# Kernel optimization log

Hardware: AMD Instinct MI355X
Metric: run time of the kernel (lower is better)

## Reference

```python
import jax, jax.numpy as jnp
import numpy as np

IN_DIMS = 4
DEPTH = 4
C = IN_DIMS + 1                     # channels after time augmentation
SIG = sum(C ** k for k in range(1, DEPTH + 1))  # 780
N, T = 64, 1024


def setup_inputs() -> dict:
    key = jax.random.key(0)
    k1, k2, k3, k4, k5 = jax.random.split(key, 5)
    batch = jax.random.normal(k1, (N, T, IN_DIMS), dtype=jnp.float32)
    s_c = 1.0 / np.sqrt(C)
    conv_w = jax.random.normal(k2, (C, C), dtype=jnp.float32) * s_c
    conv_b = jax.random.normal(k3, (C,), dtype=jnp.float32) * s_c
    s_l = 1.0 / np.sqrt(SIG)
    lin_w = jax.random.normal(k4, (SIG, SIG), dtype=jnp.float32) * s_l
    lin_b = jax.random.normal(k5, (SIG,), dtype=jnp.float32) * s_l
    return {"batch": batch, "conv_w": conv_w, "conv_b": conv_b,
            "lin_w": lin_w, "lin_b": lin_b}


def _stream_signature(path):
    """Streamed path signature with zero basepoint.

    path: (n, t, C). Returns (n, t, SIG) where entry t is the signature of
    the piecewise-linear path (0, path[0], ..., path[t]) truncated at DEPTH,
    levels flattened in lexicographic (row-major) order like signatory.
    """
    n = path.shape[0]
    # increments; basepoint=True means first increment is path[:,0] - 0
    dx = jnp.concatenate([path[:, :1, :], path[:, 1:, :] - path[:, :-1, :]], axis=1)
    init = tuple(jnp.zeros((n, C ** k), path.dtype) for k in range(1, DEPTH + 1))

    def step(levels, d):
        # exp(d) in the truncated tensor algebra: e_k = d^{(x)k} / k!
        e = [d]
        for k in range(2, DEPTH + 1):
            e.append((jnp.einsum('na,nb->nab', e[-1], d) / k).reshape(n, -1))
        # Chen: new_k = e_k + S_k + sum_{i=1}^{k-1} S_i (x) e_{k-i}
        new = []
        for k in range(1, DEPTH + 1):
            acc = levels[k - 1] + e[k - 1]
            for i in range(1, k):
                acc = acc + jnp.einsum('na,nb->nab', levels[i - 1], e[k - i - 1]).reshape(n, -1)
            new.append(acc)
        new = tuple(new)
        return new, jnp.concatenate(new, axis=-1)

    _, ys = jax.lax.scan(step, init, jnp.swapaxes(dx, 0, 1))  # ys: (t, n, SIG)
    return jnp.swapaxes(ys, 0, 1)


def reference(batch, conv_w, conv_b, lin_w, lin_b):
    n, t, _ = batch.shape
    # time augmentation: append channel arange(1,T+1)/T
    time = (jnp.arange(1, t + 1, dtype=batch.dtype) / t)[None, :, None]
    a = jnp.concatenate([batch, jnp.broadcast_to(time, (n, t, 1))], axis=-1)  # (n,t,C)
    # kernel-size-1 conv1d == pointwise linear over channels
    b = a @ conv_w.T + conv_b                                                  # (n,t,C)
    c = _stream_signature(b)                                                   # (n,t,SIG)
    # zero out the first stream entry (torch.concat of zeros with c[:,1:,:])
    c = jnp.concatenate([jnp.zeros((n, 1, SIG), c.dtype), c[:, 1:, :]], axis=1)
    return jnp.tanh(c @ lin_w.T + lin_b)
```

## Files before the change

### kernel.cpp

```cpp
#include <hip/hip_runtime.h>
#include <math.h>

#define N_B 64
#define T_LEN 1024
#define IN_D 4
#define CH 5
#define SIG 780
#define KP 800
#define NPAD 896
#define SEG_LEN 16
#define N_SEG 64
#define SC_L1 1.0f
#define SC_L2 0.25f
#define SC_L3 0.0625f
#define SC_L4 0.015625f

typedef _Float16 f16x8 __attribute__((ext_vector_type(8)));
typedef float f32x4 __attribute__((ext_vector_type(4)));

typedef __attribute__((address_space(1))) const void* as1cp;
typedef __attribute__((address_space(3))) void* as3p;

__device__ __forceinline__ float fast_tanh(float x) {
  float ax = fabsf(x);
  float e = __expf(-2.0f * ax);
  float r = (1.0f - e) * __builtin_amdgcn_rcpf(1.0f + e);
  return copysignf(r, x);
}

__device__ __forceinline__ float sel5(float d0, float d1, float d2, float d3,
                                      float d4, int i) {
  float r = d0;
  r = (i == 1) ? d1 : r;
  r = (i == 2) ? d2 : r;
  r = (i == 3) ? d3 : r;
  r = (i == 4) ? d4 : r;
  return r;
}


__global__ __launch_bounds__(64) void seg_wave(
    const float* __restrict__ batch,
    const float* __restrict__ conv_w,
    const float* __restrict__ conv_b,
    float* __restrict__ P) {
  int s = blockIdx.x;
  int n = blockIdx.y;
  int lane = threadIdx.x;

  __shared__ float S123[160];
  __shared__ float bc[85];
  __shared__ float dsh[SEG_LEN][CH];

  for (int i = lane; i < 160; i += 64) S123[i] = 0.0f;
#pragma unroll
  for (int p = 0; p < 2; ++p) {
    int e = lane + p * 64;
    if (e < (SEG_LEN + 1) * CH) {
      int r = s * SEG_LEN - 1 + e / CH, ch = e % CH;
      float v = 0.0f;
      if (r >= 0) {
        const float* a = batch + ((size_t)n * T_LEN + r) * IN_D;
        const float* w = conv_w + ch * CH;
        v = conv_b[ch];
        v = fmaf(a[0], w[0], v);
        v = fmaf(a[1], w[1], v);
        v = fmaf(a[2], w[2], v);
        v = fmaf(a[3], w[3], v);
        v = fmaf((float)(r + 1) * (1.0f / T_LEN), w[4], v);
      }
      bc[e] = v;
    }
  }
  __syncthreads();
#pragma unroll
  for (int p = 0; p < 2; ++p) {
    int e = lane + p * 64;
    if (e < SEG_LEN * CH) dsh[e / CH][e % CH] = bc[e + CH] - bc[e];
  }
  __syncthreads();

  const int xb = lane * 10;
  const int a_lo = xb / 125, a_hi = (xb + 9) / 125;
  const int s2_lo = xb / 25, s2_hi = (xb + 9) / 25;
  const int s3_lo = 2 * lane, s3_hi = 2 * lane + 1;
  const int b_lo = s2_lo % 5, b_hi = s2_hi % 5;
  const int c_lo = s3_lo % 5, c_hi = s3_hi % 5;
  const int q_a = a_lo * 125 + 125 - xb;
  const int q_b = s2_lo * 25 + 25 - xb;
  const int y0 = lane, y1 = lane + 64;
  const bool hy0 = (y0 < 125), hy1 = (y1 < 125);
  const int y0a = y0 / 25, y0s = y0 / 5, y0b = y0s % 5, y0c = y0 % 5;
  const int y1a = y1 / 25, y1s = y1 / 5, y1b = y1s % 5, y1c = y1 % 5;
  const bool hz = (lane < 25);
  const int za = lane / 5, zb = lane % 5;
  const bool h1 = (lane < 5);

  float S4r[10];
#pragma unroll
  for (int q = 0; q < 10; ++q) S4r[q] = 0.0f;

  for (int j = 0; j < SEG_LEN; ++j) {
    float dr0 = dsh[j][0], dr1 = dsh[j][1], dr2 = dsh[j][2], dr3 = dsh[j][3],
          dr4 = dsh[j][4];
    float drA[5] = {dr0, dr1, dr2, dr3, dr4};
    float da_l = sel5(dr0, dr1, dr2, dr3, dr4, a_lo);
    float da_h = sel5(dr0, dr1, dr2, dr3, dr4, a_hi);
    float db_l = sel5(dr0, dr1, dr2, dr3, dr4, b_lo);
    float db_h = sel5(dr0, dr1, dr2, dr3, dr4, b_hi);
    float dc_l = sel5(dr0, dr1, dr2, dr3, dr4, c_lo);
    float dc_h = sel5(dr0, dr1, dr2, dr3, dr4, c_hi);
    float s1_l = S123[a_lo], s1_h = S123[a_hi];
    float s2v_l = S123[5 + s2_lo], s2v_h = S123[5 + s2_hi];
    float s3v_l = S123[30 + s3_lo], s3v_h = S123[30 + s3_hi];

#pragma unroll
    for (int q = 0; q < 10; ++q) {
      bool ua = (q >= q_a), ub = (q >= q_b);
      float s1 = ua ? s1_h : s1_l, da = ua ? da_h : da_l;
      float s2v = ub ? s2v_h : s2v_l, db = ub ? db_h : db_l;
      float s3v = (q < 5) ? s3v_l : s3v_h;
      float dc = (q < 5) ? dc_l : dc_h;
      float dd = drA[q % 5];
      float tH = fmaf(0.25f, da, s1);
      tH = fmaf((1.0f / 3.0f) * db, tH, s2v);
      tH = fmaf(0.5f * dc, tH, s3v);
      S4r[q] = fmaf(dd, tH, S4r[q]);
    }

    float n3_0 = 0.f, n3_1 = 0.f, n2 = 0.f, n1 = 0.f;
    if (hy0) {
      float tH = fmaf((1.0f / 3.0f), drA[0] * 0.f + dsh[j][y0a], S123[y0a]);
      tH = fmaf(0.5f * dsh[j][y0b], tH, S123[5 + y0s]);
      n3_0 = fmaf(dsh[j][y0c], tH, S123[30 + y0]);
    }
    if (hy1) {
      float tH = fmaf((1.0f / 3.0f), dsh[j][y1a], S123[y1a]);
      tH = fmaf(0.5f * dsh[j][y1b], tH, S123[5 + y1s]);
      n3_1 = fmaf(dsh[j][y1c], tH, S123[30 + y1]);
    }
    if (hz) {
      float tH = fmaf(0.5f, dsh[j][za], S123[za]);
      n2 = fmaf(dsh[j][zb], tH, S123[5 + lane]);
    }
    if (h1) n1 = S123[lane] + dsh[j][lane];
    __syncthreads();
    if (hy0) S123[30 + y0] = n3_0;
    if (hy1) S123[30 + y1] = n3_1;
    if (hz) S123[5 + lane] = n2;
    if (h1) S123[lane] = n1;
    __syncthreads();
  }

  float* Pr = P + ((size_t)n * N_SEG + s) * SIG;
  for (int i = lane; i < 155; i += 64) Pr[i] = S123[i];
#pragma unroll
  for (int q = 0; q < 10; ++q) {
    int x = xb + q;
    if (x < 625) Pr[155 + x] = S4r[q];
  }
}

__global__ __launch_bounds__(640) void prefix_kernel(float* __restrict__ P) {
  int n = blockIdx.x;
  int tid = threadIdx.x;
  __shared__ float A[SIG];
  __shared__ float Bs[SIG];

  float* Pn = P + (size_t)n * N_SEG * SIG;
  for (int i = tid; i < SIG; i += 640) A[i] = Pn[i];
  int i0 = tid, i1 = tid + 640;
  float r0 = 0.f, r1 = 0.f;
  if (i0 < SIG) r0 = Pn[SIG + i0];
  if (i1 < SIG) r1 = Pn[SIG + i1];

  const int e4 = tid;
  const int q4a = e4 / 125, r125 = e4 % 125, r25 = e4 % 25, r5 = e4 % 5;
  const int e4d5 = e4 / 5, e4d25 = e4 / 25;
  const int e3 = tid;
  const int e3a = e3 / 25, e3r25 = e3 % 25, e3r5 = e3 % 5, e3d5 = e3 / 5;
  const int e2 = tid - 125;
  const int e1 = tid - 150;

  for (int s = 1; s < N_SEG; ++s) {
    if (i0 < SIG) Bs[i0] = r0;
    if (i1 < SIG) Bs[i1] = r1;
    __syncthreads();
    if (s + 1 < N_SEG) {
      const float* Pnx = Pn + (size_t)(s + 1) * SIG;
      if (i0 < SIG) r0 = Pnx[i0];
      if (i1 < SIG) r1 = Pnx[i1];
    }
    float v4 = 0.f, v3 = 0.f, v2 = 0.f, v1 = 0.f;
    if (tid < 625) {
      v4 = A[155 + e4] + Bs[155 + e4];
      v4 = fmaf(A[30 + e4d5], Bs[r5], v4);
      v4 = fmaf(A[5 + e4d25], Bs[5 + r25], v4);
      v4 = fmaf(A[q4a], Bs[30 + r125], v4);
    }
    if (tid < 125) {
      v3 = A[30 + e3] + Bs[30 + e3];
      v3 = fmaf(A[5 + e3d5], Bs[e3r5], v3);
      v3 = fmaf(A[e3a], Bs[5 + e3r25], v3);
    } else if (tid < 150) {
      v2 = A[5 + e2] + Bs[5 + e2];
      v2 = fmaf(A[e2 / 5], Bs[e2 % 5], v2);
    } else if (tid < 155) {
      v1 = A[e1] + Bs[e1];
    }
    __syncthreads();
    float* Po = Pn + (size_t)s * SIG;
    if (tid < 625) { A[155 + e4] = v4; Po[155 + e4] = v4; }
    if (tid < 125) { A[30 + e3] = v3; Po[30 + e3] = v3; }
    else if (tid < 150) { A[5 + e2] = v2; Po[5 + e2] = v2; }
    else if (tid < 155) { A[e1] = v1; Po[e1] = v1; }
  }
}

__global__ __launch_bounds__(64) void emit_wave(
    const float* __restrict__ batch,
    const float* __restrict__ conv_w,
    const float* __restrict__ conv_b,
    const float* __restrict__ P,
    _Float16* __restrict__ c1,
    _Float16* __restrict__ c2) {
  int s = blockIdx.x;
  int n = blockIdx.y;
  int lane = threadIdx.x;

  __shared__ float S123[160];
  __shared__ float bc[85];
  __shared__ float dsh[SEG_LEN][CH];
  __shared__ __align__(16) _Float16 row1[KP];
  __shared__ __align__(16) _Float16 row2[KP];

  const int xb = lane * 10;
  float S4r[10];
  if (s == 0) {
    for (int i = lane; i < 160; i += 64) S123[i] = 0.0f;
#pragma unroll
    for (int q = 0; q < 10; ++q) S4r[q] = 0.0f;
  } else {
    const float* Pr = P + ((size_t)n * N_SEG + (s - 1)) * SIG;
    for (int i = lane; i < 155; i += 64) S123[i] = Pr[i];
    if (lane < 5) S123[155 + lane] = 0.0f;
#pragma unroll
    for (int q = 0; q < 10; ++q) {
      int x = xb + q;
      S4r[q] = (x < 625) ? Pr[155 + x] : 0.0f;
    }
  }
#pragma unroll
  for (int p = 0; p < 2; ++p) {
    int e = lane + p * 64;
    if (e < (SEG_LEN + 1) * CH) {
      int r = s * SEG_LEN - 1 + e / CH, ch = e % CH;
      float v = 0.0f;
      if (r >= 0) {
        const float* a = batch + ((size_t)n * T_LEN + r) * IN_D;
        const float* w = conv_w + ch * CH;
        v = conv_b[ch];
        v = fmaf(a[0], w[0], v);
        v = fmaf(a[1], w[1], v);
        v = fmaf(a[2], w[2], v);
        v = fmaf(a[3], w[3], v);
        v = fmaf((float)(r + 1) * (1.0f / T_LEN), w[4], v);
      }
      bc[e] = v;
    }
  }
  if (lane < KP - SIG) {
    row1[SIG + lane] = (_Float16)0.0f;
    row2[SIG + lane] = (_Float16)0.0f;
  }
  __syncthreads();
#pragma unroll
  for (int p = 0; p < 2; ++p) {
    int e = lane + p * 64;
    if (e < SEG_LEN * CH) dsh[e / CH][e % CH] = bc[e + CH] - bc[e];
  }
  __syncthreads();

  const int a_lo = xb / 125, a_hi = (xb + 9) / 125;
  const int s2_lo = xb / 25, s2_hi = (xb + 9) / 25;
  const int s3_lo = 2 * lane, s3_hi = 2 * lane + 1;
  const int b_lo = s2_lo % 5, b_hi = s2_hi % 5;
  const int c_lo = s3_lo % 5, c_hi = s3_hi % 5;
  const int q_a = a_lo * 125 + 125 - xb;
  const int q_b = s2_lo * 25 + 25 - xb;
  const int y0 = lane, y1 = lane + 64;
  const bool hy0 = (y0 < 125), hy1 = (y1 < 125);
  const int y0a = y0 / 25, y0s = y0 / 5, y0b = y0s % 5, y0c = y0 % 5;
  const int y1a = y1 / 25, y1s = y1 / 5, y1b = y1s % 5, y1c = y1 % 5;
  const bool hz = (lane < 25);
  const int za = lane / 5, zb = lane % 5;
  const bool h1 = (lane < 5);

  for (int j = 0; j < SEG_LEN; ++j) {
    int t = s * SEG_LEN + j;
    float zf = (t == 0) ? 0.0f : 1.0f;
    float dr0 = dsh[j][0], dr1 = dsh[j][1], dr2 = dsh[j][2], dr3 = dsh[j][3],
          dr4 = dsh[j][4];
    float drA[5] = {dr0, dr1, dr2, dr3, dr4};
    float da_l = sel5(dr0, dr1, dr2, dr3, dr4, a_lo);
    float da_h = sel5(dr0, dr1, dr2, dr3, dr4, a_hi);
    float db_l = sel5(dr0, dr1, dr2, dr3, dr4, b_lo);
    float db_h = sel5(dr0, dr1, dr2, dr3, dr4, b_hi);
    float dc_l = sel5(dr0, dr1, dr2, dr3, dr4, c_lo);
    float dc_h = sel5(dr0, dr1, dr2, dr3, dr4, c_hi);
    float s1_l = S123[a_lo], s1_h = S123[a_hi];
    float s2v_l = S123[5 + s2_lo], s2v_h = S123[5 + s2_hi];
    float s3v_l = S123[30 + s3_lo], s3v_h = S123[30 + s3_hi];

#pragma unroll
    for (int q = 0; q < 10; ++q) {
      bool ua = (q >= q_a), ub = (q >= q_b);
      float s1 = ua ? s1_h : s1_l, da = ua ? da_h : da_l;
      float s2v = ub ? s2v_h : s2v_l, db = ub ? db_h : db_l;
      float s3v = (q < 5) ? s3v_l : s3v_h;
      float dc = (q < 5) ? dc_l : dc_h;
      float dd = drA[q % 5];
      float tH = fmaf(0.25f, da, s1);
      tH = fmaf((1.0f / 3.0f) * db, tH, s2v);
      tH = fmaf(0.5f * dc, tH, s3v);
      S4r[q] = fmaf(dd, tH, S4r[q]);
    }

    float n3_0 = 0.f, n3_1 = 0.f, n2 = 0.f, n1 = 0.f;
    if (hy0) {
      float tH = fmaf((1.0f / 3.0f), dsh[j][y0a], S123[y0a]);
      tH = fmaf(0.5f * dsh[j][y0b], tH, S123[5 + y0s]);
      n3_0 = fmaf(dsh[j][y0c], tH, S123[30 + y0]);
    }
    if (hy1) {
      float tH = fmaf((1.0f / 3.0f), dsh[j][y1a], S123[y1a]);
      tH = fmaf(0.5f * dsh[j][y1b], tH, S123[5 + y1s]);
      n3_1 = fmaf(dsh[j][y1c], tH, S123[30 + y1]);
    }
    if (hz) {
      float tH = fmaf(0.5f, dsh[j][za], S123[za]);
      n2 = fmaf(dsh[j][zb], tH, S123[5 + lane]);
    }
    if (h1) n1 = S123[lane] + dsh[j][lane];
    __syncthreads();

    if (hy0) S123[30 + y0] = n3_0;
    if (hy1) S123[30 + y1] = n3_1;
    if (hz) S123[5 + lane] = n2;
    if (h1) S123[lane] = n1;
#pragma unroll
    for (int q = 0; q < 10; ++q) {
      int x = xb + q;
      if (x < 625) {
        float v = S4r[q] * (SC_L4 * zf);
        _Float16 h = (_Float16)v;
        row1[155 + x] = h;
        row2[155 + x] = (_Float16)(v - (float)h);
      }
    }
    if (hy0) {
      float v = n3_0 * (SC_L3 * zf);
      _Float16 h = (_Float16)v;
      row1[30 + y0] = h; row2[30 + y0] = (_Float16)(v - (float)h);
    }
    if (hy1) {
      float v = n3_1 * (SC_L3 * zf);
      _Float16 h = (_Float16)v;
      row1[30 + y1] = h; row2[30 + y1] = (_Float16)(v - (float)h);
    }
    if (hz) {
      float v = n2 * (SC_L2 * zf);
      _Float16 h = (_Float16)v;
      row1[5 + lane] = h; row2[5 + lane] = (_Float16)(v - (float)h);
    }
    if (h1) {
      float v = n1 * (SC_L1 * zf);
      _Float16 h = (_Float16)v;
      row1[lane] = h; row2[lane] = (_Float16)(v - (float)h);
    }
    __syncthreads();

    size_t base = ((size_t)n * T_LEN + t) * KP;
    *(float4*)(c1 + base + lane * 8) = *(const float4*)&row1[lane * 8];
    *(float4*)(c2 + base + lane * 8) = *(const float4*)&row2[lane * 8];
    if (lane < 36) {
      *(float4*)(c1 + base + (64 + lane) * 8) = *(const float4*)&row1[(64 + lane) * 8];
      *(float4*)(c2 + base + (64 + lane) * 8) = *(const float4*)&row2[(64 + lane) * 8];
    }
  }
}

__global__ __launch_bounds__(256) void wconv_kernel(
    const float* __restrict__ W,
    _Float16* __restrict__ w1,
    _Float16* __restrict__ w2) {
  int idx = blockIdx.x * blockDim.x + threadIdx.x;
  if (idx >= NPAD * KP) return;
  int nn = idx / KP, k = idx % KP;
  float v = 0.0f;
  if (nn < SIG && k < SIG) {
    float sc = (k < 5) ? 1.0f : (k < 30) ? 4.0f : (k < 155) ? 16.0f : 64.0f;
    v = W[(size_t)nn * SIG + k] * sc;
  }
  _Float16 h = (_Float16)v;
  w1[idx] = h;
  w2[idx] = (_Float16)(v - (float)h);
}

__global__ __launch_bounds__(256) void gemm_mfma(
    const _Float16* __restrict__ A1p, const _Float16* __restrict__ A2p,
    const _Float16* __restrict__ B1p, const _Float16* __restrict__ B2p,
    const float* __restrict__ bias, float* __restrict__ out) {
  __shared__ _Float16 Al[2][2][128 * 32];
  __shared__ _Float16 Bl[2][2][128 * 32];

  int tid = threadIdx.x;
  int lane = tid & 63, wid = tid >> 6;
  int wm = wid >> 1, wn = wid & 1;
  int m0 = blockIdx.x * 128;

  int sr = lane >> 2, scn = lane & 3;
  int swst = (sr ^ (sr >> 2)) & 3;
  int qg = scn ^ swst;
  int fr = lane & 15, fq = lane >> 4;
  int swf = (fr ^ (fr >> 2)) & 3;
  int fchunk = fq ^ swf;

  auto stage = [&](int n0, int kb, int buf) {
    int k0 = kb * 32;
#pragma unroll
    for (int i = 0; i < 2; ++i) {
      int rloc = wid * 16 + i * 64 + sr;
      size_t gA = (size_t)(m0 + rloc) * KP + k0 + qg * 8;
      size_t gB = (size_t)(n0 + rloc) * KP + k0 + qg * 8;
      int lb = (wid * 16 + i * 64) * 32;
      __builtin_amdgcn_global_load_lds((as1cp)(A1p + gA), (as3p)(&Al[buf][0][lb]), 16, 0, 0);
      __builtin_amdgcn_global_load_lds((as1cp)(A2p + gA), (as3p)(&Al[buf][1][lb]), 16, 0, 0);
      __builtin_amdgcn_global_load_lds((as1cp)(B1p + gB), (as3p)(&Bl[buf][0][lb]), 16, 0, 0);
      __builtin_amdgcn_global_load_lds((as1cp)(B2p + gB), (as3p)(&Bl[buf][1][lb]), 16, 0, 0);
    }
  };

  for (int nt = 0; nt < 7; ++nt) {
    int n0 = nt * 128;

    f32x4 acc[4][4];
#pragma unroll
    for (int i = 0; i < 4; ++i)
#pragma unroll
      for (int j = 0; j < 4; ++j) acc[i][j] = (f32x4){0.f, 0.f, 0.f, 0.f};

    stage(n0, 0, 0);
    for (int kb = 0; kb < 25; ++kb) {
      int cur = kb & 1;
      __syncthreads();
      f16x8 a1[4], a2[4], b1[4], b2[4];
#pragma unroll
      for (int tm = 0; tm < 4; ++tm) {
        int off = (wm * 64 + tm * 16 + fr) * 32 + fchunk * 8;
        a1[tm] = *(const f16x8*)&Al[cur][0][off];
        a2[tm] = *(const f16x8*)&Al[cur][1][off];
      }
#pragma unroll
      for (int tn = 0; tn < 4; ++tn) {
        int off = (wn * 64 + tn * 16 + fr) * 32 + fchunk * 8;
        b1[tn] = *(const f16x8*)&Bl[cur][0][off];
        b2[tn] = *(const f16x8*)&Bl[cur][1][off];
      }
      if (kb < 24) stage(n0, kb + 1, cur ^ 1);
#pragma unroll
      for (int tm = 0; tm < 4; ++tm)
#pragma unroll
        for (int tn = 0; tn < 4; ++tn) {
          acc[tm][tn] = __builtin_amdgcn_mfma_f32_16x16x32_f16(a1[tm], b1[tn], acc[tm][tn], 0, 0, 0);
          acc[tm][tn] = __builtin_amdgcn_mfma_f32_16x16x32_f16(a1[tm], b2[tn], acc[tm][tn], 0, 0, 0);
          acc[tm][tn] = __builtin_amdgcn_mfma_f32_16x16x32_f16(a2[tm], b1[tn], acc[tm][tn], 0, 0, 0);
        }
    }
    __syncthreads();

    float* ep = (float*)((wid < 2) ? (void*)&Al[0][0][0] : (void*)&Bl[0][0][0]);
    ep += (wid & 1) * 4096;

    float bv[4];
#pragma unroll
    for (int tn = 0; tn < 4; ++tn) {
      int nn = n0 + wn * 64 + tn * 16 + fr;
      bv[tn] = (nn < SIG) ? bias[nn] : 0.0f;
    }
#pragma unroll
    for (int h = 0; h < 2; ++h) {
#pragma unroll
      for (int tm2 = 0; tm2 < 2; ++tm2) {
        int tm = h * 2 + tm2;
#pragma unroll
        for (int tn = 0; tn < 4; ++tn) {
#pragma unroll
          for (int r = 0; r < 4; ++r) {
            int lr = tm2 * 16 + fq * 4 + r;
            int lc = tn * 16 + fr;
            ep[lr * 66 + lc] = fast_tanh(acc[tm][tn][r] + bv[tn]);
          }
        }
      }
#pragma unroll
      for (int p = 0; p < 2; ++p) {
        int lr = lane & 31;
        int ck = (lane >> 5) * 2 + p;
        int gm = m0 + wm * 64 + h * 32 + lr;
        int gc0 = n0 + wn * 64 + ck * 16;
#pragma unroll
        for (int q = 0; q < 4; ++q) {
          int col = gc0 + q * 4;
          if (col + 3 < SIG) {
            *(float4*)(out + (size_t)gm * SIG + col) =
                *(const float4*)&ep[lr * 66 + ck * 16 + q * 4];
          } else if (col < SIG) {
#pragma unroll
            for (int e = 0; e < 4; ++e) {
              int c2 = col + e;
              if (c2 < SIG) out[(size_t)gm * SIG + c2] = ep[lr * 66 + ck * 16 + q * 4 + e];
            }
          }
        }
      }
    }
    __syncthreads();
  }
}

__global__ __launch_bounds__(256) void conv_kernel(
    const float* __restrict__ batch,
    const float* __restrict__ conv_w,
    const float* __restrict__ conv_b,
    float* __restrict__ b_out) {
  int idx = blockIdx.x * blockDim.x + threadIdx.x;
  if (idx >= N_B * T_LEN) return;
  int t = idx & (T_LEN - 1);
  const float* a = batch + (size_t)idx * IN_D;
  float a0 = a[0], a1 = a[1], a2 = a[2], a3 = a[3];
  float tm = (float)(t + 1) / (float)T_LEN;
  float* o = b_out + (size_t)idx * CH;
#pragma unroll
  for (int j = 0; j < CH; ++j) {
    const float* w = conv_w + j * CH;
    float r = conv_b[j];
    r = fmaf(tm, w[4], r);
    r = fmaf(a3, w[3], r);
    r = fmaf(a2, w[2], r);
    r = fmaf(a1, w[1], r);
    r = fmaf(a0, w[0], r);
    o[j] = r;
  }
}

__global__ __launch_bounds__(320) void sig_kernel_fb(
    const float* __restrict__ b_in, float* __restrict__ c_out) {
  int n = blockIdx.x;
  int tid = threadIdx.x;
  __shared__ float S[SIG];
  __shared__ float bc[64 * CH];
  __shared__ float dsh[CH];
  __shared__ float pb[CH];
  for (int i = tid; i < SIG; i += 320) S[i] = 0.0f;
  if (tid < CH) pb[tid] = 0.0f;
  const float* bn = b_in + (size_t)n * T_LEN * CH;
  float* cn = c_out + (size_t)n * T_LEN * SIG;
  const int x0 = tid, x1 = tid + 320;
  const bool has1 = (tid < 305);
  const int a0i = x0 / 125, b0i = (x0 / 25) % 5, c0i = (x0 / 5) % 5, d0i = x0 % 5;
  const int a1i = x1 / 125, b1i = (x1 / 25) % 5, c1i = (x1 / 5) % 5, d1i = x1 % 5;
  const int s2_0 = x0 / 25, s3_0 = x0 / 5, s2_1 = x1 / 25, s3_1 = x1 / 5;
  const bool hasL3 = (tid < 125);
  const int ya = tid / 25, yb = (tid / 5) % 5, yc = tid % 5;
  const bool hasL2 = (tid < 25);
  const int za = tid / 5, zb = tid % 5;
  const bool hasL1 = (tid < CH);
  for (int t = 0; t < T_LEN; ++t) {
    if ((t & 63) == 0) {
      __syncthreads();
      bc[tid] = bn[t * CH + tid];
      __syncthreads();
    }
    if (tid < CH) {
      float cur = bc[(t & 63) * CH + tid];
      dsh[tid] = cur - pb[tid];
      pb[tid] = cur;
    }
    __syncthreads();
    float n4_0, n4_1 = 0.0f, n3 = 0.0f, n2 = 0.0f, n1 = 0.0f;
    {
      float tH = fmaf(0.25f, dsh[a0i], S[a0i]);
      tH = fmaf((1.0f / 3.0f) * dsh[b0i], tH, S[5 + s2_0]);
      tH = fmaf(0.5f * dsh[c0i], tH, S[30 + s3_0]);
      n4_0 = fmaf(dsh[d0i], tH, S[155 + x0]);
    }
    if (has1) {
      float tH = fmaf(0.25f, dsh[a1i], S[a1i]);
      tH = fmaf((1.0f / 3.0f) * dsh[b1i], tH, S[5 + s2_1]);
      tH = fmaf(0.5f * dsh[c1i], tH, S[30 + s3_1]);
      n4_1 = fmaf(dsh[d1i], tH, S[155 + x1]);
    }
    if (hasL3) {
      float tH = fmaf((1.0f / 3.0f), dsh[ya], S[ya]);
      tH = fmaf(0.5f * dsh[yb], tH, S[5 + ya * 5 + yb]);
      n3 = fmaf(dsh[yc], tH, S[30 + tid]);
    }
    if (hasL2) {
      float tH = fmaf(0.5f, dsh[za], S[za]);
      n2 = fmaf(dsh[zb], tH, S[5 + tid]);
    }
    if (hasL1) n1 = S[tid] + dsh[tid];
    __syncthreads();
    S[155 + x0] = n4_0;
    if (has1) S[155 + x1] = n4_1;
    if (hasL3) S[30 + tid] = n3;
    if (hasL2) S[5 + tid] = n2;
    if (hasL1) S[tid] = n1;
    float* crow = cn + (size_t)t * SIG;
    float z = (t == 0) ? 0.0f : 1.0f;
    crow[155 + x0] = n4_0 * z;
    if (has1) crow[155 + x1] = n4_1 * z;
    if (hasL3) crow[30 + tid] = n3 * z;
    if (hasL2) crow[5 + tid] = n2 * z;
    if (hasL1) crow[tid] = n1 * z;
    __syncthreads();
  }
}

#define BM 256
#define BN 64
#define BK 16
__global__ __launch_bounds__(256) void gemm_tanh_fb(
    const float* __restrict__ Cmat, const float* __restrict__ W,
    const float* __restrict__ bias, float* __restrict__ out) {
  __shared__ float As[BK][BM + 4];
  __shared__ float Ws[BK][BN + 4];
  int tid = threadIdx.x;
  int tx = tid & 7, ty = tid >> 3;
  int m0 = blockIdx.x * BM, n0 = blockIdx.y * BN;
  float acc[8][8];
#pragma unroll
  for (int i = 0; i < 8; ++i)
#pragma unroll
    for (int j = 0; j < 8; ++j) acc[i][j] = 0.0f;
  for (int kb = 0; kb < SIG; kb += BK) {
    __syncthreads();
#pragma unroll
    for (int p = 0; p < 4; ++p) {
      int id = tid + p * 256;
      int row = id >> 2, kg = (id & 3) * 4, gk = kb + kg;
      float4 v = make_float4(0.f, 0.f, 0.f, 0.f);
      if (gk < SIG) v = *(const float4*)(Cmat + (size_t)(m0 + row) * SIG + gk);
      As[kg + 0][row] = v.x; As[kg + 1][row] = v.y;
      As[kg + 2][row] = v.z; As[kg + 3][row] = v.w;
    }
    {
      int row = tid >> 2, kg = (tid & 3) * 4, gk = kb + kg, wr = n0 + row;
      float4 v = make_float4(0.f, 0.f, 0.f, 0.f);
      if (gk < SIG && wr < SIG) v = *(const float4*)(W + (size_t)wr * SIG + gk);
      Ws[kg + 0][row] = v.x; Ws[kg + 1][row] = v.y;
      Ws[kg + 2][row] = v.z; Ws[kg + 3][row] = v.w;
    }
    __syncthreads();
#pragma unroll
    for (int k = 0; k < BK; ++k) {
      float af[8], wf[8];
      *(float4*)&af[0] = *(const float4*)&As[k][ty * 8];
      *(float4*)&af[4] = *(const float4*)&As[k][ty * 8 + 4];
      *(float4*)&wf[0] = *(const float4*)&Ws[k][tx * 8];
      *(float4*)&wf[4] = *(const float4*)&Ws[k][tx * 8 + 4];
#pragma unroll
      for (int i = 0; i < 8; ++i)
#pragma unroll
        for (int j = 0; j < 8; ++j) acc[i][j] = fmaf(af[i], wf[j], acc[i][j]);
    }
  }
#pragma unroll
  for (int i = 0; i < 8; ++i) {
    int m = m0 + ty * 8 + i;
    float* orow = out + (size_t)m * SIG;
#pragma unroll
    for (int jj = 0; jj < 8; jj += 4) {
      int col = n0 + tx * 8 + jj;
      if (col < SIG) {
        float4 r;
        r.x = tanhf(acc[i][jj + 0] + bias[col + 0]);
        r.y = tanhf(acc[i][jj + 1] + bias[col + 1]);
        r.z = tanhf(acc[i][jj + 2] + bias[col + 2]);
        r.w = tanhf(acc[i][jj + 3] + bias[col + 3]);
        *(float4*)(orow + col) = r;
      }
    }
  }
}

extern "C" void kernel_launch(void* const* d_in, const int* in_sizes, int n_in,
                              void* d_out, int out_size, void* d_ws, size_t ws_size,
                              hipStream_t stream) {
  const float* batch = (const float*)d_in[0];
  const float* conv_w = (const float*)d_in[1];
  const float* conv_b = (const float*)d_in[2];
  const float* lin_w = (const float*)d_in[3];
  const float* lin_b = (const float*)d_in[4];
  float* out = (float*)d_out;

  const size_t plane_elems = (size_t)N_B * T_LEN * KP;
  const size_t wplane_elems = (size_t)NPAD * KP;
  const size_t P_elems = (size_t)N_B * N_SEG * SIG;
  const size_t bp_elems = (size_t)N_B * T_LEN * CH;
  const size_t need_big = 2 * plane_elems * sizeof(_Float16) +
                          2 * wplane_elems * sizeof(_Float16) +
                          P_elems * sizeof(float);

  if (ws_size >= need_big) {
    _Float16* c1 = (_Float16*)d_ws;
    _Float16* c2 = c1 + plane_elems;
    _Float16* w1 = c2 + plane_elems;
    _Float16* w2 = w1 + wplane_elems;
    float* P = (float*)(w2 + wplane_elems);

    wconv_kernel<<<dim3((NPAD * KP + 255) / 256), dim3(256), 0, stream>>>(
        lin_w, w1, w2);
    seg_wave<<<dim3(N_SEG, N_B), dim3(64), 0, stream>>>(batch, conv_w, conv_b, P);
    prefix_kernel<<<dim3(N_B), dim3(640), 0, stream>>>(P);
    emit_wave<<<dim3(N_SEG, N_B), dim3(64), 0, stream>>>(
        batch, conv_w, conv_b, P, c1, c2);
    gemm_mfma<<<dim3(512), dim3(256), 0, stream>>>(c1, c2, w1, w2, lin_b, out);
  } else {
    float* b_path = (float*)d_ws;
    float* c_sig = (float*)d_ws + bp_elems;
    conv_kernel<<<dim3((N_B * T_LEN + 255) / 256), dim3(256), 0, stream>>>(
        batch, conv_w, conv_b, b_path);
    sig_kernel_fb<<<dim3(N_B), dim3(320), 0, stream>>>(b_path, c_sig);
    gemm_tanh_fb<<<dim3((N_B * T_LEN) / BM, (SIG + BN - 1) / BN), dim3(256), 0, stream>>>(
        c_sig, lin_w, lin_b, out);
  }
}
```

Before: 733.1 us.

## Pre-swizzle GEMM operands into MFMA fragment order and load directly to registers

emit_wave now buffers 16 timestep rows in LDS and writes the A operands (hi/lo f16 splits) in a blocked, MFMA-fragment-ordered layout. The weight conversion kernel writes B in the same order. The GEMM becomes gemm_direct: 3584 blocks, each computing one 128x128 output tile, loading fragments straight from global into registers with a software double buffer instead of staging through LDS with barriers. It also uses launch_bounds(256,2) and remaps blocks for locality. This removes LDS staging and syncs in the GEMM, but depends on global/L2 latency being hidden by the register double buffer, and raises emit_wave's LDS use.

```diff
diff --git a/kernel.cpp b/kernel.cpp
--- a/kernel.cpp
+++ b/kernel.cpp
@@ -10,6 +10,7 @@
 #define NPAD 896
 #define SEG_LEN 16
 #define N_SEG 64
+#define GBLK 51200
 #define SC_L1 1.0f
 #define SC_L2 0.25f
 #define SC_L3 0.0625f
@@ -17,9 +18,6 @@
 
 typedef _Float16 f16x8 __attribute__((ext_vector_type(8)));
 typedef float f32x4 __attribute__((ext_vector_type(4)));
-
-typedef __attribute__((address_space(1))) const void* as1cp;
-typedef __attribute__((address_space(3))) void* as3p;
 
 __device__ __forceinline__ float fast_tanh(float x) {
   float ax = fabsf(x);
@@ -37,7 +35,6 @@
   r = (i == 4) ? d4 : r;
   return r;
 }
-
 
 __global__ __launch_bounds__(64) void seg_wave(
     const float* __restrict__ batch,
@@ -130,7 +127,7 @@
 
     float n3_0 = 0.f, n3_1 = 0.f, n2 = 0.f, n1 = 0.f;
     if (hy0) {
-      float tH = fmaf((1.0f / 3.0f), drA[0] * 0.f + dsh[j][y0a], S123[y0a]);
+      float tH = fmaf((1.0f / 3.0f), dsh[j][y0a], S123[y0a]);
       tH = fmaf(0.5f * dsh[j][y0b], tH, S123[5 + y0s]);
       n3_0 = fmaf(dsh[j][y0c], tH, S123[30 + y0]);
     }
@@ -231,8 +228,7 @@
   __shared__ float S123[160];
   __shared__ float bc[85];
   __shared__ float dsh[SEG_LEN][CH];
-  __shared__ __align__(16) _Float16 row1[KP];
-  __shared__ __align__(16) _Float16 row2[KP];
+  __shared__ __align__(16) _Float16 rowbuf[2][16][808];
 
   const int xb = lane * 10;
   float S4r[10];
@@ -269,9 +265,9 @@
       bc[e] = v;
     }
   }
-  if (lane < KP - SIG) {
-    row1[SIG + lane] = (_Float16)0.0f;
-    row2[SIG + lane] = (_Float16)0.0f;
+  for (int i = lane; i < 2 * 16 * 20; i += 64) {
+    int p = i / 320, rr = (i / 20) % 16, cc = i % 20;
+    rowbuf[p][rr][780 + cc] = (_Float16)0.0f;
   }
   __syncthreads();
 #pragma unroll
@@ -348,184 +344,197 @@
     if (hy1) S123[30 + y1] = n3_1;
     if (hz) S123[5 + lane] = n2;
     if (h1) S123[lane] = n1;
+    _Float16* r1 = &rowbuf[0][j][0];
+    _Float16* r2 = &rowbuf[1][j][0];
 #pragma unroll
     for (int q = 0; q < 10; ++q) {
       int x = xb + q;
       if (x < 625) {
         float v = S4r[q] * (SC_L4 * zf);
         _Float16 h = (_Float16)v;
-        row1[155 + x] = h;
-        row2[155 + x] = (_Float16)(v - (float)h);
+        r1[155 + x] = h;
+        r2[155 + x] = (_Float16)(v - (float)h);
       }
     }
     if (hy0) {
       float v = n3_0 * (SC_L3 * zf);
       _Float16 h = (_Float16)v;
-      row1[30 + y0] = h; row2[30 + y0] = (_Float16)(v - (float)h);
+      r1[30 + y0] = h; r2[30 + y0] = (_Float16)(v - (float)h);
     }
     if (hy1) {
       float v = n3_1 * (SC_L3 * zf);
       _Float16 h = (_Float16)v;
-      row1[30 + y1] = h; row2[30 + y1] = (_Float16)(v - (float)h);
+      r1[30 + y1] = h; r2[30 + y1] = (_Float16)(v - (float)h);
     }
     if (hz) {
       float v = n2 * (SC_L2 * zf);
       _Float16 h = (_Float16)v;
-      row1[5 + lane] = h; row2[5 + lane] = (_Float16)(v - (float)h);
+      r1[5 + lane] = h; r2[5 + lane] = (_Float16)(v - (float)h);
     }
     if (h1) {
       float v = n1 * (SC_L1 * zf);
       _Float16 h = (_Float16)v;
-      row1[lane] = h; row2[lane] = (_Float16)(v - (float)h);
-    }
-    __syncthreads();
-
-    size_t base = ((size_t)n * T_LEN + t) * KP;
-    *(float4*)(c1 + base + lane * 8) = *(const float4*)&row1[lane * 8];
-    *(float4*)(c2 + base + lane * 8) = *(const float4*)&row2[lane * 8];
-    if (lane < 36) {
-      *(float4*)(c1 + base + (64 + lane) * 8) = *(const float4*)&row1[(64 + lane) * 8];
-      *(float4*)(c2 + base + (64 + lane) * 8) = *(const float4*)&row2[(64 + lane) * 8];
-    }
-  }
-}
-
-__global__ __launch_bounds__(256) void wconv_kernel(
+      r1[lane] = h; r2[lane] = (_Float16)(v - (float)h);
+    }
+    __syncthreads();
+  }
+
+  {
+    int g = n * 16 + (s >> 2);
+    int tm_r = s & 3;
+    int frl = lane & 15, fql = lane >> 4;
+    _Float16* d1 = c1 + (size_t)g * GBLK + tm_r * 512 + lane * 8;
+    _Float16* d2 = c2 + (size_t)g * GBLK + tm_r * 512 + lane * 8;
+#pragma unroll
+    for (int kb = 0; kb < 25; ++kb) {
+      *(f16x8*)(d1 + kb * 2048) = *(const f16x8*)&rowbuf[0][frl][kb * 32 + fql * 8];
+      *(f16x8*)(d2 + kb * 2048) = *(const f16x8*)&rowbuf[1][frl][kb * 32 + fql * 8];
+    }
+  }
+}
+
+__global__ __launch_bounds__(256) void wswz_kernel(
     const float* __restrict__ W,
     _Float16* __restrict__ w1,
     _Float16* __restrict__ w2) {
   int idx = blockIdx.x * blockDim.x + threadIdx.x;
-  if (idx >= NPAD * KP) return;
-  int nn = idx / KP, k = idx % KP;
+  if (idx >= 14 * GBLK) return;
+  int gn = idx / GBLK;
+  int r1 = idx % GBLK;
+  int kb = r1 / 2048;
+  int r2 = r1 % 2048;
+  int tn = r2 / 512;
+  int r3 = r2 % 512;
+  int fq = r3 / 128;
+  int fr = (r3 >> 3) & 15;
+  int jv = r3 & 7;
+  int nrow = gn * 64 + tn * 16 + fr;
+  int k = kb * 32 + fq * 8 + jv;
   float v = 0.0f;
-  if (nn < SIG && k < SIG) {
+  if (nrow < SIG && k < SIG) {
     float sc = (k < 5) ? 1.0f : (k < 30) ? 4.0f : (k < 155) ? 16.0f : 64.0f;
-    v = W[(size_t)nn * SIG + k] * sc;
+    v = W[(size_t)nrow * SIG + k] * sc;
   }
   _Float16 h = (_Float16)v;
   w1[idx] = h;
   w2[idx] = (_Float16)(v - (float)h);
 }
 
-__global__ __launch_bounds__(256) void gemm_mfma(
+__global__ __launch_bounds__(256, 2) void gemm_direct(
     const _Float16* __restrict__ A1p, const _Float16* __restrict__ A2p,
     const _Float16* __restrict__ B1p, const _Float16* __restrict__ B2p,
     const float* __restrict__ bias, float* __restrict__ out) {
-  __shared__ _Float16 Al[2][2][128 * 32];
-  __shared__ _Float16 Bl[2][2][128 * 32];
+  __shared__ float eplds[4][2112];
 
   int tid = threadIdx.x;
   int lane = tid & 63, wid = tid >> 6;
   int wm = wid >> 1, wn = wid & 1;
-  int m0 = blockIdx.x * 128;
-
-  int sr = lane >> 2, scn = lane & 3;
-  int swst = (sr ^ (sr >> 2)) & 3;
-  int qg = scn ^ swst;
+  int b = blockIdx.x;
+  int x = b & 7, jj = b >> 3;
+  int mstrip = x * 64 + jj / 7;
+  int nt = jj % 7;
+
+  int g = mstrip * 2 + wm;
+  int gn = nt * 2 + wn;
+
+  const _Float16* aB1 = A1p + (size_t)g * GBLK + lane * 8;
+  const _Float16* aB2 = A2p + (size_t)g * GBLK + lane * 8;
+  const _Float16* bB1 = B1p + (size_t)gn * GBLK + lane * 8;
+  const _Float16* bB2 = B2p + (size_t)gn * GBLK + lane * 8;
+
+  f32x4 acc[4][4];
+#pragma unroll
+  for (int i = 0; i < 4; ++i)
+#pragma unroll
+    for (int j = 0; j < 4; ++j) acc[i][j] = (f32x4){0.f, 0.f, 0.f, 0.f};
+
+  f16x8 aE1[4], aE2[4], bE1[4], bE2[4];
+  f16x8 aO1[4], aO2[4], bO1[4], bO2[4];
+
+  auto loadf = [&](int kb, f16x8* A1f, f16x8* A2f, f16x8* B1f, f16x8* B2f) {
+    int o = kb * 2048;
+#pragma unroll
+    for (int tt = 0; tt < 4; ++tt) {
+      A1f[tt] = *(const f16x8*)(aB1 + o + tt * 512);
+      A2f[tt] = *(const f16x8*)(aB2 + o + tt * 512);
+      B1f[tt] = *(const f16x8*)(bB1 + o + tt * 512);
+      B2f[tt] = *(const f16x8*)(bB2 + o + tt * 512);
+    }
+  };
+  auto domfma = [&](f16x8* A1f, f16x8* A2f, f16x8* B1f, f16x8* B2f) {
+#pragma unroll
+    for (int tm = 0; tm < 4; ++tm)
+#pragma unroll
+      for (int tn = 0; tn < 4; ++tn)
+        acc[tm][tn] = __builtin_amdgcn_mfma_f32_16x16x32_f16(A1f[tm], B1f[tn], acc[tm][tn], 0, 0, 0);
+#pragma unroll
+    for (int tm = 0; tm < 4; ++tm)
+#pragma unroll
+      for (int tn = 0; tn < 4; ++tn)
+        acc[tm][tn] = __builtin_amdgcn_mfma_f32_16x16x32_f16(A1f[tm], B2f[tn], acc[tm][tn], 0, 0, 0);
+#pragma unroll
+    for (int tm = 0; tm < 4; ++tm)
+#pragma unroll
+      for (int tn = 0; tn < 4; ++tn)
+        acc[tm][tn] = __builtin_amdgcn_mfma_f32_16x16x32_f16(A2f[tm], B1f[tn], acc[tm][tn], 0, 0, 0);
+  };
+
+  loadf(0, aE1, aE2, bE1, bE2);
+#pragma unroll 1
+  for (int i = 0; i < 12; ++i) {
+    loadf(2 * i + 1, aO1, aO2, bO1, bO2);
+    domfma(aE1, aE2, bE1, bE2);
+    loadf(2 * i + 2, aE1, aE2, bE1, bE2);
+    domfma(aO1, aO2, bO1, bO2);
+  }
+  domfma(aE1, aE2, bE1, bE2);
+
+  int m0 = mstrip * 128, n0 = nt * 128;
   int fr = lane & 15, fq = lane >> 4;
-  int swf = (fr ^ (fr >> 2)) & 3;
-  int fchunk = fq ^ swf;
-
-  auto stage = [&](int n0, int kb, int buf) {
-    int k0 = kb * 32;
-#pragma unroll
-    for (int i = 0; i < 2; ++i) {
-      int rloc = wid * 16 + i * 64 + sr;
-      size_t gA = (size_t)(m0 + rloc) * KP + k0 + qg * 8;
-      size_t gB = (size_t)(n0 + rloc) * KP + k0 + qg * 8;
-      int lb = (wid * 16 + i * 64) * 32;
-      __builtin_amdgcn_global_load_lds((as1cp)(A1p + gA), (as3p)(&Al[buf][0][lb]), 16, 0, 0);
-      __builtin_amdgcn_global_load_lds((as1cp)(A2p + gA), (as3p)(&Al[buf][1][lb]), 16, 0, 0);
-      __builtin_amdgcn_global_load_lds((as1cp)(B1p + gB), (as3p)(&Bl[buf][0][lb]), 16, 0, 0);
-      __builtin_amdgcn_global_load_lds((as1cp)(B2p + gB), (as3p)(&Bl[buf][1][lb]), 16, 0, 0);
-    }
-  };
-
-  for (int nt = 0; nt < 7; ++nt) {
-    int n0 = nt * 128;
-
-    f32x4 acc[4][4];
-#pragma unroll
-    for (int i = 0; i < 4; ++i)
-#pragma unroll
-      for (int j = 0; j < 4; ++j) acc[i][j] = (f32x4){0.f, 0.f, 0.f, 0.f};
-
-    stage(n0, 0, 0);
-    for (int kb = 0; kb < 25; ++kb) {
-      int cur = kb & 1;
-      __syncthreads();
-      f16x8 a1[4], a2[4], b1[4], b2[4];
-#pragma unroll
-      for (int tm = 0; tm < 4; ++tm) {
-        int off = (wm * 64 + tm * 16 + fr) * 32 + fchunk * 8;
-        a1[tm] = *(const f16x8*)&Al[cur][0][off];
-        a2[tm] = *(const f16x8*)&Al[cur][1][off];
+  float* ep = eplds[wid];
+
+  float bv[4];
+#pragma unroll
+  for (int tn = 0; tn < 4; ++tn) {
+    int nn = n0 + wn * 64 + tn * 16 + fr;
+    bv[tn] = (nn < SIG) ? bias[nn] : 0.0f;
+  }
+#pragma unroll
+  for (int h = 0; h < 2; ++h) {
+#pragma unroll
+    for (int tm2 = 0; tm2 < 2; ++tm2) {
+      int tm = h * 2 + tm2;
+#pragma unroll
+      for (int tn = 0; tn < 4; ++tn) {
+#pragma unroll
+        for (int r = 0; r < 4; ++r) {
+          int lr = tm2 * 16 + fq * 4 + r;
+          int lc = tn * 16 + fr;
+          ep[lr * 66 + lc] = fast_tanh(acc[tm][tn][r] + bv[tn]);
+        }
       }
-#pragma unroll
-      for (int tn = 0; tn < 4; ++tn) {
-        int off = (wn * 64 + tn * 16 + fr) * 32 + fchunk * 8;
-        b1[tn] = *(const f16x8*)&Bl[cur][0][off];
-        b2[tn] = *(const f16x8*)&Bl[cur][1][off];
-      }
-      if (kb < 24) stage(n0, kb + 1, cur ^ 1);
-#pragma unroll
-      for (int tm = 0; tm < 4; ++tm)
-#pragma unroll
-        for (int tn = 0; tn < 4; ++tn) {
-          acc[tm][tn] = __builtin_amdgcn_mfma_f32_16x16x32_f16(a1[tm], b1[tn], acc[tm][tn], 0, 0, 0);
-          acc[tm][tn] = __builtin_amdgcn_mfma_f32_16x16x32_f16(a1[tm], b2[tn], acc[tm][tn], 0, 0, 0);
-          acc[tm][tn] = __builtin_amdgcn_mfma_f32_16x16x32_f16(a2[tm], b1[tn], acc[tm][tn], 0, 0, 0);
-        }
-    }
-    __syncthreads();
-
-    float* ep = (float*)((wid < 2) ? (void*)&Al[0][0][0] : (void*)&Bl[0][0][0]);
-    ep += (wid & 1) * 4096;
-
-    float bv[4];
-#pragma unroll
-    for (int tn = 0; tn < 4; ++tn) {
-      int nn = n0 + wn * 64 + tn * 16 + fr;
-      bv[tn] = (nn < SIG) ? bias[nn] : 0.0f;
-    }
-#pragma unroll
-    for (int h = 0; h < 2; ++h) {
-#pragma unroll
-      for (int tm2 = 0; tm2 < 2; ++tm2) {
-        int tm = h * 2 + tm2;
-#pragma unroll
-        for (int tn = 0; tn < 4; ++tn) {
-#pragma unroll
-          for (int r = 0; r < 4; ++r) {
-            int lr = tm2 * 16 + fq * 4 + r;
-            int lc = tn * 16 + fr;
-            ep[lr * 66 + lc] = fast_tanh(acc[tm][tn][r] + bv[tn]);
+    }
+#pragma unroll
+    for (int p = 0; p < 2; ++p) {
+      int lr = lane & 31;
+      int ck = (lane >> 5) * 2 + p;
+      int gm = m0 + wm * 64 + h * 32 + lr;
+      int gc0 = n0 + wn * 64 + ck * 16;
+#pragma unroll
+      for (int q = 0; q < 4; ++q) {
+        int col = gc0 + q * 4;
+        if (col + 3 < SIG) {
+          *(float4*)(out + (size_t)gm * SIG + col) =
+              *(const float4*)&ep[lr * 66 + ck * 16 + q * 4];
+        } else if (col < SIG) {
+#pragma unroll
+          for (int e = 0; e < 4; ++e) {
+            int c2 = col + e;
+            if (c2 < SIG) out[(size_t)gm * SIG + c2] = ep[lr * 66 + ck * 16 + q * 4 + e];
           }
         }
       }
-#pragma unroll
-      for (int p = 0; p < 2; ++p) {
-        int lr = lane & 31;
-        int ck = (lane >> 5) * 2 + p;
-        int gm = m0 + wm * 64 + h * 32 + lr;
-        int gc0 = n0 + wn * 64 + ck * 16;
-#pragma unroll
-        for (int q = 0; q < 4; ++q) {
-          int col = gc0 + q * 4;
-          if (col + 3 < SIG) {
-            *(float4*)(out + (size_t)gm * SIG + col) =
-                *(const float4*)&ep[lr * 66 + ck * 16 + q * 4];
-          } else if (col < SIG) {
-#pragma unroll
-            for (int e = 0; e < 4; ++e) {
-              int c2 = col + e;
-              if (c2 < SIG) out[(size_t)gm * SIG + c2] = ep[lr * 66 + ck * 16 + q * 4 + e];
-            }
-          }
-        }
-      }
-    }
-    __syncthreads();
+    }
   }
 }
 
@@ -720,13 +729,13 @@
     _Float16* w2 = w1 + wplane_elems;
     float* P = (float*)(w2 + wplane_elems);
 
-    wconv_kernel<<<dim3((NPAD * KP + 255) / 256), dim3(256), 0, stream>>>(
+    wswz_kernel<<<dim3((14 * GBLK + 255) / 256), dim3(256), 0, stream>>>(
         lin_w, w1, w2);
     seg_wave<<<dim3(N_SEG, N_B), dim3(64), 0, stream>>>(batch, conv_w, conv_b, P);
     prefix_kernel<<<dim3(N_B), dim3(640), 0, stream>>>(P);
     emit_wave<<<dim3(N_SEG, N_B), dim3(64), 0, stream>>>(
         batch, conv_w, conv_b, P, c1, c2);
-    gemm_mfma<<<dim3(512), dim3(256), 0, stream>>>(c1, c2, w1, w2, lin_b, out);
+    gemm_direct<<<dim3(3584), dim3(256), 0, stream>>>(c1, c2, w1, w2, lin_b, out);
   } else {
     float* b_path = (float*)d_ws;
     float* c_sig = (float*)d_ws + bp_elems;
```

New measurement: 762.4 us. +4.0%, slower.
